# Kernel optimization log

Hardware: AMD Instinct MI355X
Metric: run time of the kernel (lower is better)

Reference implementation:

```python
import jax, jax.numpy as jnp
import numpy as np


def setup_inputs() -> dict:
    key = jax.random.key(0)
    ks = jax.random.split(key, 5)
    B, T, C, HS = 8, 2048, 1024, 64
    return {
        "x_q": jax.random.normal(ks[0], (B, T, C), dtype=jnp.float32),
        "x_kv": jax.random.normal(ks[1], (B, T, C), dtype=jnp.float32),
        "Wq": jax.random.normal(ks[2], (C, HS), dtype=jnp.float32) * (C ** -0.5),
        "Wk": jax.random.normal(ks[3], (C, HS), dtype=jnp.float32) * (C ** -0.5),
        "Wv": jax.random.normal(ks[4], (C, HS), dtype=jnp.float32) * (C ** -0.5),
    }


def reference(x_q, x_kv, Wq, Wk, Wv):
    # x_q, x_kv: [B, T, C]; W*: [C, HS]
    B, T, C = x_q.shape
    q = jnp.einsum("btc,ch->bth", x_q, Wq)   # [B, T, HS]
    k = jnp.einsum("btc,ch->bth", x_kv, Wk)  # [B, T, HS]
    v = jnp.einsum("btc,ch->bth", x_kv, Wv)  # [B, T, HS]
    # NOTE: original scales by d_model**-0.5 (C), not head_size**-0.5
    wei = jnp.einsum("bqh,bkh->bqk", q, k) * (C ** -0.5)  # [B, T, T]
    causal = jnp.tril(jnp.ones((T, T), dtype=bool))
    wei = jnp.where(causal, wei, -jnp.inf)
    wei = jax.nn.softmax(wei, axis=-1)
    out = jnp.einsum("bqk,bkh->bqh", wei, v)  # [B, T, HS]
    return out
```

## Files before the change

### kernel.cpp

```cpp
#include <hip/hip_runtime.h>

typedef __bf16 bf16_t;
typedef __bf16 bf16x8 __attribute__((ext_vector_type(8)));
typedef float f32x4 __attribute__((ext_vector_type(4)));
typedef unsigned short u16x4 __attribute__((ext_vector_type(4)));

#define B_ 8
#define T_ 2048
#define C_ 1024
#define HS_ 64

#define MFMA __builtin_amdgcn_mfma_f32_16x16x32_bf16

__device__ __forceinline__ float fast_exp2(float x) {
#if __has_builtin(__builtin_amdgcn_exp2f)
  return __builtin_amdgcn_exp2f(x);
#else
  return exp2f(x);
#endif
}

__global__ __launch_bounds__(256) void repack_w(
    const float* __restrict__ Wq, const float* __restrict__ Wk,
    const float* __restrict__ Wv, bf16_t* __restrict__ pq,
    bf16_t* __restrict__ pk, bf16_t* __restrict__ pv) {
  const float* W = (blockIdx.y == 0) ? Wq : ((blockIdx.y == 1) ? Wk : Wv);
  bf16_t* P = (blockIdx.y == 0) ? pq : ((blockIdx.y == 1) ? pk : pv);
  int t = blockIdx.x * 256 + threadIdx.x;
  int lane = t & 63, nt = (t >> 6) & 3, kc = t >> 8;
  int quad = lane >> 4, ln = lane & 15;
  bf16x8 v;
#pragma unroll
  for (int j = 0; j < 8; ++j)
    v[j] = (bf16_t)W[(kc * 32 + quad * 8 + j) * HS_ + nt * 16 + ln];
  *(bf16x8*)(P + (size_t)t * 8) = v;
}

__global__ __launch_bounds__(512) void proj_mfma(
    const float* __restrict__ xq, const float* __restrict__ xkv,
    const bf16_t* __restrict__ pq, const bf16_t* __restrict__ pk,
    const bf16_t* __restrict__ pv, bf16_t* __restrict__ q,
    bf16_t* __restrict__ k, bf16_t* __restrict__ vT) {
  __shared__ float r0[4][16][68];
  __shared__ float r1[4][16][68];

  const int rt = blockIdx.x;
  const bool is_kv = (blockIdx.y != 0);
  const int wv = threadIdx.x >> 6, lane = threadIdx.x & 63;
  const int wr = wv & 3, kh = wv >> 2;
  const int quad = lane >> 4, ln = lane & 15;
  const int m0 = rt * 64 + wr * 16;
  const float* x = is_kv ? xkv : xq;
  const bf16_t* p0 = is_kv ? pk : pq;

  f32x4 acc0[4], acc1[4];
#pragma unroll
  for (int nt = 0; nt < 4; ++nt) {
    acc0[nt] = (f32x4){0.f, 0.f, 0.f, 0.f};
    acc1[nt] = (f32x4){0.f, 0.f, 0.f, 0.f};
  }

  for (int kc = kh * 16; kc < kh * 16 + 16; ++kc) {
    const float* xf = x + (size_t)(m0 + ln) * C_ + kc * 32 + quad * 8;
    f32x4 lo = *(const f32x4*)xf;
    f32x4 hi = *(const f32x4*)(xf + 4);
    bf16x8 a;
#pragma unroll
    for (int j = 0; j < 4; ++j) {
      a[j] = (bf16_t)lo[j];
      a[4 + j] = (bf16_t)hi[j];
    }
#pragma unroll
    for (int nt = 0; nt < 4; ++nt) {
      bf16x8 b = *(const bf16x8*)(p0 + ((size_t)(kc * 4 + nt) * 64 + lane) * 8);
      acc0[nt] = MFMA(a, b, acc0[nt], 0, 0, 0);
    }
    if (is_kv) {
#pragma unroll
      for (int nt = 0; nt < 4; ++nt) {
        bf16x8 b = *(const bf16x8*)(pv + ((size_t)(kc * 4 + nt) * 64 + lane) * 8);
        acc1[nt] = MFMA(a, b, acc1[nt], 0, 0, 0);
      }
    }
  }

  if (kh == 1) {
#pragma unroll
    for (int nt = 0; nt < 4; ++nt)
#pragma unroll
      for (int r = 0; r < 4; ++r) {
        r0[wr][quad * 4 + r][nt * 16 + ln] = acc0[nt][r];
        if (is_kv) r1[wr][quad * 4 + r][nt * 16 + ln] = acc1[nt][r];
      }
  }
  __syncthreads();
  if (kh != 0) return;

#pragma unroll
  for (int nt = 0; nt < 4; ++nt)
#pragma unroll
    for (int r = 0; r < 4; ++r) {
      acc0[nt][r] += r0[wr][quad * 4 + r][nt * 16 + ln];
      if (is_kv) acc1[nt][r] += r1[wr][quad * 4 + r][nt * 16 + ln];
    }

  if (!is_kv) {
#pragma unroll
    for (int nt = 0; nt < 4; ++nt)
#pragma unroll
      for (int r = 0; r < 4; ++r)
        q[(size_t)(m0 + quad * 4 + r) * HS_ + nt * 16 + ln] = (bf16_t)acc0[nt][r];
  } else {
#pragma unroll
    for (int nt = 0; nt < 4; ++nt)
#pragma unroll
      for (int r = 0; r < 4; ++r)
        k[(size_t)(m0 + quad * 4 + r) * HS_ + nt * 16 + ln] = (bf16_t)acc0[nt][r];
    const int bb = m0 >> 11, t0 = m0 & (T_ - 1);
#pragma unroll
    for (int nt = 0; nt < 4; ++nt) {
      u16x4 pk4;
#pragma unroll
      for (int r = 0; r < 4; ++r) {
        bf16_t h = (bf16_t)acc1[nt][r];
        pk4[r] = *(unsigned short*)&h;
      }
      *(u16x4*)((unsigned short*)vT + ((size_t)(bb * HS_ + nt * 16 + ln)) * T_ +
                t0 + quad * 4) = pk4;
    }
  }
}

__global__ __launch_bounds__(512) void attn_mfma(
    const bf16_t* __restrict__ q, const bf16_t* __restrict__ k,
    const bf16_t* __restrict__ vT, float* __restrict__ out) {
  __shared__ bf16_t p_lds[8][16][80];
  __shared__ float o_buf[7][16][68];
  __shared__ float l_buf[8][16][16];

  const int b = blockIdx.x >> 7;
  const int gq = blockIdx.x & 127;
  const int w = threadIdx.x >> 6, lane = threadIdx.x & 63;
  const int quad = lane >> 4, ln = lane & 15;
  const int qr0 = gq * 16;
  const size_t bt = (size_t)b * T_;
  const int td = gq >> 2;

  bf16x8 aq[2];
#pragma unroll
  for (int hc = 0; hc < 2; ++hc)
    aq[hc] = *(const bf16x8*)(q + (bt + qr0 + ln) * HS_ + hc * 32 + quad * 8);

  f32x4 o_acc[4];
  float l_part[4] = {0.f, 0.f, 0.f, 0.f};
#pragma unroll
  for (int nt = 0; nt < 4; ++nt) o_acc[nt] = (f32x4){0.f, 0.f, 0.f, 0.f};
  const float scl = 0.03125f * 1.44269504088896340736f;

  for (int t = w; t <= td; t += 8) {
    const int kr0 = t * 64;

    f32x4 s[4];
#pragma unroll
    for (int nt = 0; nt < 4; ++nt) s[nt] = (f32x4){0.f, 0.f, 0.f, 0.f};
#pragma unroll
    for (int hc = 0; hc < 2; ++hc)
#pragma unroll
      for (int nt = 0; nt < 4; ++nt) {
        bf16x8 bk = *(const bf16x8*)(k + (bt + kr0 + nt * 16 + ln) * HS_ +
                                     hc * 32 + quad * 8);
        s[nt] = MFMA(aq[hc], bk, s[nt], 0, 0, 0);
      }

    const bool diag = (t == td);
#pragma unroll
    for (int nt = 0; nt < 4; ++nt)
#pragma unroll
      for (int r = 0; r < 4; ++r) {
        float e = fast_exp2(s[nt][r] * scl);
        if (diag && (kr0 + nt * 16 + ln > qr0 + quad * 4 + r)) e = 0.f;
        l_part[r] += e;
        p_lds[w][quad * 4 + r][nt * 16 + ln] = (bf16_t)e;
      }

#pragma unroll
    for (int kc = 0; kc < 2; ++kc) {
      bf16x8 ap = *(const bf16x8*)&p_lds[w][ln][kc * 32 + quad * 8];
#pragma unroll
      for (int nt = 0; nt < 4; ++nt) {
        bf16x8 bv = *(const bf16x8*)(vT + ((size_t)(b * HS_ + nt * 16 + ln)) * T_ +
                                     kr0 + kc * 32 + quad * 8);
        o_acc[nt] = MFMA(ap, bv, o_acc[nt], 0, 0, 0);
      }
    }
  }

  if (w != 0) {
#pragma unroll
    for (int nt = 0; nt < 4; ++nt)
#pragma unroll
      for (int r = 0; r < 4; ++r)
        o_buf[w - 1][quad * 4 + r][nt * 16 + ln] = o_acc[nt][r];
  }
#pragma unroll
  for (int r = 0; r < 4; ++r) l_buf[w][quad * 4 + r][ln] = l_part[r];
  __syncthreads();

  if (w == 0) {
#pragma unroll
    for (int ww = 0; ww < 7; ++ww)
#pragma unroll
      for (int nt = 0; nt < 4; ++nt)
#pragma unroll
        for (int r = 0; r < 4; ++r)
          o_acc[nt][r] += o_buf[ww][quad * 4 + r][nt * 16 + ln];
    float l_row[4];
#pragma unroll
    for (int r = 0; r < 4; ++r) {
      float v = 0.f;
#pragma unroll
      for (int ww = 0; ww < 8; ++ww) v += l_buf[ww][quad * 4 + r][ln];
#pragma unroll
      for (int off = 1; off < 16; off <<= 1) v += __shfl_xor(v, off);
      l_row[r] = v;
    }
#pragma unroll
    for (int nt = 0; nt < 4; ++nt)
#pragma unroll
      for (int r = 0; r < 4; ++r)
        out[(bt + qr0 + quad * 4 + r) * HS_ + nt * 16 + ln] =
            o_acc[nt][r] / l_row[r];
  }
}

extern "C" void kernel_launch(void* const* d_in, const int* in_sizes, int n_in,
                              void* d_out, int out_size, void* d_ws,
                              size_t ws_size, hipStream_t stream) {
  (void)in_sizes; (void)n_in; (void)out_size; (void)ws_size;
  const float* xq = (const float*)d_in[0];
  const float* xkv = (const float*)d_in[1];
  const float* Wq = (const float*)d_in[2];
  const float* Wk = (const float*)d_in[3];
  const float* Wv = (const float*)d_in[4];
  float* out = (float*)d_out;

  char* ws = (char*)d_ws;
  bf16_t* q = (bf16_t*)ws;
  bf16_t* kk = (bf16_t*)(ws + (2u << 20));
  bf16_t* vT = (bf16_t*)(ws + (4u << 20));
  bf16_t* pq = (bf16_t*)(ws + (6u << 20));
  bf16_t* pk = (bf16_t*)(ws + (6u << 20) + (128u << 10));
  bf16_t* pv = (bf16_t*)(ws + (6u << 20) + (256u << 10));

  repack_w<<<dim3(32, 3), 256, 0, stream>>>(Wq, Wk, Wv, pq, pk, pv);
  proj_mfma<<<dim3(256, 2), 512, 0, stream>>>(xq, xkv, pq, pk, pv, q, kk, vT);
  attn_mfma<<<dim3(1024), 512, 0, stream>>>(q, kk, vT, out);
}
```

Before: 221.4 us.

## Parallelize attention epilogue reduction across waves and batch projection loads

The attention epilogue now has all eight waves write their partial O and row-sum to LDS, and every wave reduces two rows, instead of wave 0 doing the whole reduction serially. LDS padding changes to 66/17 to alter bank mapping. In the projection kernel the K-loop is unrolled by four so eight global fp32 loads are issued before the conversions and MFMAs, giving more memory-level parallelism. The cost is higher register pressure in the projection and somewhat more LDS for o_buf.

Measured after the change: 219.7 us. Within noise of the previous version (-0.7%).

```diff
diff --git a/kernel.cpp b/kernel.cpp
--- a/kernel.cpp
+++ b/kernel.cpp
@@ -41,8 +41,8 @@
     const bf16_t* __restrict__ pq, const bf16_t* __restrict__ pk,
     const bf16_t* __restrict__ pv, bf16_t* __restrict__ q,
     bf16_t* __restrict__ k, bf16_t* __restrict__ vT) {
-  __shared__ float r0[4][16][68];
-  __shared__ float r1[4][16][68];
+  __shared__ float r0[4][16][66];
+  __shared__ float r1[4][16][66];
 
   const int rt = blockIdx.x;
   const bool is_kv = (blockIdx.y != 0);
@@ -60,26 +60,35 @@
     acc1[nt] = (f32x4){0.f, 0.f, 0.f, 0.f};
   }
 
-  for (int kc = kh * 16; kc < kh * 16 + 16; ++kc) {
-    const float* xf = x + (size_t)(m0 + ln) * C_ + kc * 32 + quad * 8;
-    f32x4 lo = *(const f32x4*)xf;
-    f32x4 hi = *(const f32x4*)(xf + 4);
-    bf16x8 a;
-#pragma unroll
-    for (int j = 0; j < 4; ++j) {
-      a[j] = (bf16_t)lo[j];
-      a[4 + j] = (bf16_t)hi[j];
-    }
-#pragma unroll
-    for (int nt = 0; nt < 4; ++nt) {
-      bf16x8 b = *(const bf16x8*)(p0 + ((size_t)(kc * 4 + nt) * 64 + lane) * 8);
-      acc0[nt] = MFMA(a, b, acc0[nt], 0, 0, 0);
-    }
-    if (is_kv) {
+  for (int kc = kh * 16; kc < kh * 16 + 16; kc += 4) {
+    f32x4 lo[4], hi[4];
+#pragma unroll
+    for (int u = 0; u < 4; ++u) {
+      const float* xf = x + (size_t)(m0 + ln) * C_ + (kc + u) * 32 + quad * 8;
+      lo[u] = *(const f32x4*)xf;
+      hi[u] = *(const f32x4*)(xf + 4);
+    }
+#pragma unroll
+    for (int u = 0; u < 4; ++u) {
+      bf16x8 a;
+#pragma unroll
+      for (int j = 0; j < 4; ++j) {
+        a[j] = (bf16_t)lo[u][j];
+        a[4 + j] = (bf16_t)hi[u][j];
+      }
 #pragma unroll
       for (int nt = 0; nt < 4; ++nt) {
-        bf16x8 b = *(const bf16x8*)(pv + ((size_t)(kc * 4 + nt) * 64 + lane) * 8);
-        acc1[nt] = MFMA(a, b, acc1[nt], 0, 0, 0);
+        bf16x8 b =
+            *(const bf16x8*)(p0 + ((size_t)((kc + u) * 4 + nt) * 64 + lane) * 8);
+        acc0[nt] = MFMA(a, b, acc0[nt], 0, 0, 0);
+      }
+      if (is_kv) {
+#pragma unroll
+        for (int nt = 0; nt < 4; ++nt) {
+          bf16x8 b =
+              *(const bf16x8*)(pv + ((size_t)((kc + u) * 4 + nt) * 64 + lane) * 8);
+          acc1[nt] = MFMA(a, b, acc1[nt], 0, 0, 0);
+        }
       }
     }
   }
@@ -135,8 +144,8 @@
     const bf16_t* __restrict__ q, const bf16_t* __restrict__ k,
     const bf16_t* __restrict__ vT, float* __restrict__ out) {
   __shared__ bf16_t p_lds[8][16][80];
-  __shared__ float o_buf[7][16][68];
-  __shared__ float l_buf[8][16][16];
+  __shared__ float o_buf[8][16][66];
+  __shared__ float l_buf[8][16][17];
 
   const int b = blockIdx.x >> 7;
   const int gq = blockIdx.x & 127;
@@ -195,41 +204,27 @@
     }
   }
 
-  if (w != 0) {
-#pragma unroll
-    for (int nt = 0; nt < 4; ++nt)
-#pragma unroll
-      for (int r = 0; r < 4; ++r)
-        o_buf[w - 1][quad * 4 + r][nt * 16 + ln] = o_acc[nt][r];
-  }
+#pragma unroll
+  for (int nt = 0; nt < 4; ++nt)
+#pragma unroll
+    for (int r = 0; r < 4; ++r)
+      o_buf[w][quad * 4 + r][nt * 16 + ln] = o_acc[nt][r];
 #pragma unroll
   for (int r = 0; r < 4; ++r) l_buf[w][quad * 4 + r][ln] = l_part[r];
   __syncthreads();
 
-  if (w == 0) {
-#pragma unroll
-    for (int ww = 0; ww < 7; ++ww)
-#pragma unroll
-      for (int nt = 0; nt < 4; ++nt)
-#pragma unroll
-        for (int r = 0; r < 4; ++r)
-          o_acc[nt][r] += o_buf[ww][quad * 4 + r][nt * 16 + ln];
-    float l_row[4];
-#pragma unroll
-    for (int r = 0; r < 4; ++r) {
-      float v = 0.f;
-#pragma unroll
-      for (int ww = 0; ww < 8; ++ww) v += l_buf[ww][quad * 4 + r][ln];
-#pragma unroll
-      for (int off = 1; off < 16; off <<= 1) v += __shfl_xor(v, off);
-      l_row[r] = v;
-    }
-#pragma unroll
-    for (int nt = 0; nt < 4; ++nt)
-#pragma unroll
-      for (int r = 0; r < 4; ++r)
-        out[(bt + qr0 + quad * 4 + r) * HS_ + nt * 16 + ln] =
-            o_acc[nt][r] / l_row[r];
+#pragma unroll
+  for (int rr = 0; rr < 2; ++rr) {
+    const int row = w + rr * 8;
+    float o = 0.f, lsum = 0.f;
+#pragma unroll
+    for (int ww = 0; ww < 8; ++ww) {
+      o += o_buf[ww][row][lane];
+      lsum += l_buf[ww][row][lane & 15];
+    }
+#pragma unroll
+    for (int off = 1; off < 16; off <<= 1) lsum += __shfl_xor(lsum, off);
+    out[(bt + qr0 + row) * HS_ + lane] = o / lsum;
   }
 }
 
```
